# Performance work log

Measured on AMD Instinct MI355X. Metric: run time of the kernel, lower is better.

Reference implementation:

```python
import jax, jax.numpy as jnp
import numpy as np

B, L, S, T_IP = 2, 4096, 77, 16
C, C_CROSS, H = 1280, 768, 20
DH = C // H
REGION_WEIGHT = 0.3  # scalar inside weight_func: bias = region_state * sigma * REGION_WEIGHT
IP_SCALE = 1.0


def setup_inputs() -> dict:
    key = jax.random.key(0)
    ks = jax.random.split(key, 11)
    def w(k, shape, s=0.02):
        return jax.random.normal(k, shape, dtype=jnp.float32) * s
    return {
        "hidden_states": jax.random.normal(ks[0], (B, L, C), dtype=jnp.float32),
        "encoder_hidden_states": jax.random.normal(ks[1], (B, S, C_CROSS), dtype=jnp.float32),
        "ip_hidden_states": jax.random.normal(ks[2], (B, T_IP, C_CROSS), dtype=jnp.float32),
        "region_state": jax.random.uniform(ks[3], (B, L, S), dtype=jnp.float32),
        "sigma": jnp.full((1,), 14.6, dtype=jnp.float32),
        "Wq": w(ks[4], (C, C)),
        "Wk": w(ks[5], (C_CROSS, C)),
        "Wv": w(ks[6], (C_CROSS, C)),
        "Wk_ip": w(ks[7], (C_CROSS, C)),
        "Wv_ip": w(ks[8], (C_CROSS, C)),
        "Wout": w(ks[9], (C, C)),
        "b_out": jnp.zeros((C,), dtype=jnp.float32),
    }


def _split_heads(x):
    # [B, T, C] -> [B, H, T, DH]
    b, t, _ = x.shape
    return x.reshape(b, t, H, DH).transpose(0, 2, 1, 3)


def reference(hidden_states, encoder_hidden_states, ip_hidden_states, region_state,
              sigma, Wq, Wk, Wv, Wk_ip, Wv_ip, Wout, b_out):
    residual = hidden_states
    scale = 1.0 / np.sqrt(DH).astype(np.float32)

    q = _split_heads(hidden_states @ Wq)            # [B,H,L,DH]
    k = _split_heads(encoder_hidden_states @ Wk)    # [B,H,S,DH]
    v = _split_heads(encoder_hidden_states @ Wv)    # [B,H,S,DH]

    # region-state-biased cross attention (manual softmax path)
    scores = jnp.einsum('bhld,bhsd->bhls', q, k) * scale  # [B,H,L,S]
    # weight_func(region_state, sigma, attn_weight) -> region_state * sigma * REGION_WEIGHT,
    # broadcast over heads (repeat_interleave B -> B*H in the original).
    bias = (region_state * sigma[0] * REGION_WEIGHT)[:, None, :, :]  # [B,1,L,S]
    attn = jax.nn.softmax(scores + bias, axis=-1)
    out = jnp.einsum('bhls,bhsd->bhld', attn, v)
    out = out.transpose(0, 2, 1, 3).reshape(B, L, C)

    # IP-adapter stream: standard SDPA against image-prompt tokens
    k_ip = _split_heads(ip_hidden_states @ Wk_ip)   # [B,H,T,DH]
    v_ip = _split_heads(ip_hidden_states @ Wv_ip)
    s_ip = jax.nn.softmax(jnp.einsum('bhld,bhtd->bhlt', q, k_ip) * scale, axis=-1)
    out_ip = jnp.einsum('bhlt,bhtd->bhld', s_ip, v_ip).transpose(0, 2, 1, 3).reshape(B, L, C)

    out = out + IP_SCALE * out_ip
    out = out @ Wout + b_out     # attn.to_out[0]; to_out[1] is dropout (identity at p=0)
    return out + residual
```

## Files before the change

kernel.cpp:

```cpp
#include <hip/hip_runtime.h>
#include <cstdint>
#include <cstddef>

#define B_   2
#define L_   4096
#define S_   77
#define TIP_ 16
#define C_   1280
#define CC_  768
#define H_   20

typedef unsigned short u16;
typedef unsigned int   u32;
typedef __attribute__((ext_vector_type(8))) short bf16x8;
typedef __attribute__((ext_vector_type(8))) unsigned short u16x8;
typedef __attribute__((ext_vector_type(4))) float f32x4;

__device__ __forceinline__ u16 f2bf(float x) {
  u32 u = __float_as_uint(x);
  u32 r = (u + 0x7fffu + ((u >> 16) & 1u)) >> 16;
  return (u16)r;
}

__device__ __forceinline__ void gload16(const u16* g, const u16* l) {
  __builtin_amdgcn_global_load_lds(
      (const __attribute__((address_space(1))) u32*)g,
      (__attribute__((address_space(3))) u32*)(uintptr_t)l, 16, 0, 0);
}

__device__ __forceinline__ void wg_barrier() {
  asm volatile("s_barrier" ::: "memory");
}
template<int N>
__device__ __forceinline__ void vm_wait() {
  asm volatile("s_waitcnt vmcnt(%0)" :: "i"(N) : "memory");
}

__global__ __launch_bounds__(256) void prep_cast(
    const float* __restrict__ X, const float* __restrict__ enc, const float* __restrict__ ip,
    u16* __restrict__ Xbf, u16* __restrict__ encbf, u16* __restrict__ ipbf) {
  const int nX = B_*L_*C_;
  const int nE = B_*S_*CC_;
  const int nI = B_*TIP_*CC_;
  const int total4 = (nX + nE + nI) >> 2;
  for (int i = blockIdx.x*256 + threadIdx.x; i < total4; i += gridDim.x*256) {
    int idx = i << 2;
    const float* src; u16* dst; int off;
    if (idx < nX)            { src = X;   dst = Xbf;   off = idx; }
    else if (idx < nX + nE)  { src = enc; dst = encbf; off = idx - nX; }
    else                     { src = ip;  dst = ipbf;  off = idx - nX - nE; }
    float4 v = *(const float4*)(src + off);
    ushort4 o;
    o.x = f2bf(v.x); o.y = f2bf(v.y); o.z = f2bf(v.z); o.w = f2bf(v.w);
    *(ushort4*)(dst + off) = o;
  }
}

__global__ __launch_bounds__(256) void transpose_cast(
    const float* __restrict__ Wq,  const float* __restrict__ Wk,   const float* __restrict__ Wv,
    const float* __restrict__ Wkip,const float* __restrict__ Wvip, const float* __restrict__ Wout,
    u16* __restrict__ WqT, u16* __restrict__ WkT, u16* __restrict__ WvT,
    u16* __restrict__ WkipT, u16* __restrict__ WvipT, u16* __restrict__ WoutT) {
  const int m = blockIdx.y;
  const float* src; u16* dst; int K;
  switch (m) {
    case 0: src = Wq;   dst = WqT;   K = C_;  break;
    case 1: src = Wk;   dst = WkT;   K = CC_; break;
    case 2: src = Wv;   dst = WvT;   K = CC_; break;
    case 3: src = Wkip; dst = WkipT; K = CC_; break;
    case 4: src = Wvip; dst = WvipT; K = CC_; break;
    default:src = Wout; dst = WoutT; K = C_;  break;
  }
  const int tileK = blockIdx.x / 40;
  const int tileN = blockIdx.x % 40;
  if (tileK >= (K >> 5)) return;
  __shared__ float tile[32][33];
  const int tx = threadIdx.x & 31, ty = threadIdx.x >> 5;
  const int k0 = tileK*32, n0 = tileN*32;
  #pragma unroll
  for (int r = 0; r < 32; r += 8)
    tile[ty + r][tx] = src[(size_t)(k0 + ty + r)*C_ + n0 + tx];
  __syncthreads();
  #pragma unroll
  for (int r = 0; r < 32; r += 8) {
    const int n = n0 + ty + r, k = k0 + tx;
    dst[(size_t)n*K + k] = f2bf(tile[tx][ty + r]);
  }
}

template<int BN, int MODE, typename OutT>
__device__ __forceinline__ void gemm_core(
    const u16* __restrict__ A, int lda, int M,
    const u16* __restrict__ BT, int K,
    OutT* __restrict__ Cm,
    const float* __restrict__ bias, const float* __restrict__ resid,
    int mt, int nt) {
  constexpr int NF  = BN / 32;
  constexpr int BCH = BN / 32;
  constexpr int LP  = 4 + BCH;
  __shared__ u16 As0[128*64];
  __shared__ u16 Bs0[BN*64];
  __shared__ u16 As1[128*64];
  __shared__ u16 Bs1[BN*64];
  const int tid  = threadIdx.x;
  const int lane = tid & 63, wave = tid >> 6;
  const int wm = wave >> 1, wn = wave & 1;
  const int lhi = lane >> 4, llo = lane & 15;
  const int lsw = llo & 7;

  f32x4 acc[4][NF] = {};

  auto stage = [&](int kt, u16* As, u16* Bs) {
    #pragma unroll
    for (int it = 0; it < 4; ++it) {
      const int chunk = it*256 + wave*64 + lane;
      const int r  = chunk >> 3;
      const int c8 = chunk & 7;
      const int g8 = c8 ^ (r & 7);
      int row_g = mt*128 + r; row_g = (row_g < M) ? row_g : (M - 1);
      gload16(A + (size_t)row_g*lda + kt*64 + g8*8,
              As + (size_t)(it*256 + wave*64)*8);
    }
    #pragma unroll
    for (int it = 0; it < BCH; ++it) {
      const int chunk = it*256 + wave*64 + lane;
      const int r  = chunk >> 3;
      const int c8 = chunk & 7;
      const int g8 = c8 ^ (r & 7);
      const int nrow = nt*BN + r;
      gload16(BT + (size_t)nrow*K + kt*64 + g8*8,
              Bs + (size_t)(it*256 + wave*64)*8);
    }
  };

  auto compute = [&](const u16* As, const u16* Bs) {
    #pragma unroll
    for (int ks = 0; ks < 2; ++ks) {
      bf16x8 av[4], bv[NF];
      #pragma unroll
      for (int mm = 0; mm < 4; ++mm) {
        const int row = wm*64 + mm*16 + llo;
        av[mm] = *(const bf16x8*)(As + row*64 + (((ks*4 + lhi) ^ lsw) << 3));
      }
      #pragma unroll
      for (int nn = 0; nn < NF; ++nn) {
        const int row = wn*(BN/2) + nn*16 + llo;
        bv[nn] = *(const bf16x8*)(Bs + row*64 + (((ks*4 + lhi) ^ lsw) << 3));
      }
      #pragma unroll
      for (int mm = 0; mm < 4; ++mm)
        #pragma unroll
        for (int nn = 0; nn < NF; ++nn)
          acc[mm][nn] = __builtin_amdgcn_mfma_f32_16x16x32_bf16(av[mm], bv[nn], acc[mm][nn], 0, 0, 0);
    }
  };

  const int nkt = K >> 6;
  stage(0, As0, Bs0);
  stage(1, As1, Bs1);
  vm_wait<LP>();
  wg_barrier();
  __builtin_amdgcn_sched_barrier(0);

  for (int kt = 0; kt < nkt; ++kt) {
    u16* As = (kt & 1) ? As1 : As0;
    u16* Bs = (kt & 1) ? Bs1 : Bs0;
    compute(As, Bs);
    if (kt + 2 < nkt) {
      wg_barrier();
      stage(kt + 2, As, Bs);
      vm_wait<LP>();
      wg_barrier();
      __builtin_amdgcn_sched_barrier(0);
    } else if (kt + 1 < nkt) {
      vm_wait<0>();
      wg_barrier();
      __builtin_amdgcn_sched_barrier(0);
    }
  }

  #pragma unroll
  for (int mm = 0; mm < 4; ++mm) {
    #pragma unroll
    for (int nn = 0; nn < NF; ++nn) {
      const int row0 = mt*128 + wm*64 + mm*16 + lhi*4;
      const int col  = nt*BN + wn*(BN/2) + nn*16 + llo;
      #pragma unroll
      for (int r = 0; r < 4; ++r) {
        const int row = row0 + r;
        if (row < M) {
          float v = acc[mm][nn][r];
          if constexpr (MODE == 1) {
            v += bias[col] + resid[(size_t)row*C_ + col];
            Cm[(size_t)row*C_ + col] = v;
          } else {
            Cm[(size_t)row*C_ + col] = f2bf(v);
          }
        }
      }
    }
  }
}

template<int MODE, typename OutT>
__global__ __launch_bounds__(256, 2) void gemm_bf16(
    const u16* __restrict__ A, int lda, int M, const u16* __restrict__ BT, int K,
    OutT* __restrict__ Cm, const float* __restrict__ bias, const float* __restrict__ resid) {
  const int nwg = gridDim.x;
  const int bid = blockIdx.x;
  const int swz = (nwg & 7) ? bid : ((bid & 7) * (nwg >> 3) + (bid >> 3));
  gemm_core<160, MODE, OutT>(A, lda, M, BT, K, Cm, bias, resid, swz >> 3, swz & 7);
}

__global__ __launch_bounds__(256, 2) void gemm_small(
    const u16* __restrict__ encbf, const u16* __restrict__ ipbf,
    const u16* __restrict__ WkT, const u16* __restrict__ WvT,
    const u16* __restrict__ WkipT, const u16* __restrict__ WvipT,
    u16* __restrict__ Kbf, u16* __restrict__ Vbf,
    u16* __restrict__ Kipbf, u16* __restrict__ Vipbf) {
  const int z = blockIdx.y;
  const u16* A; const u16* BT; u16* Cm; int M;
  if      (z == 0) { A = encbf; BT = WkT;   Cm = Kbf;   M = B_*S_; }
  else if (z == 1) { A = encbf; BT = WvT;   Cm = Vbf;   M = B_*S_; }
  else if (z == 2) { A = ipbf;  BT = WkipT; Cm = Kipbf; M = B_*TIP_; }
  else             { A = ipbf;  BT = WvipT; Cm = Vipbf; M = B_*TIP_; }
  gemm_core<128, 2, u16>(A, CC_, M, BT, CC_, Cm, nullptr, nullptr, blockIdx.x / 10, blockIdx.x % 10);
}

#define KSP   96
#define KLD   72
#define PLD   104
__global__ __launch_bounds__(256) void attn_mfma(
    const u16* __restrict__ Qbf,
    const u16* __restrict__ Kbf,  const u16* __restrict__ Vbf,
    const u16* __restrict__ Kipbf, const u16* __restrict__ Vipbf,
    const float* __restrict__ region, const float* __restrict__ sigma,
    u16* __restrict__ attnbf) {
  __shared__ u16 Kl[KSP*KLD];
  __shared__ u16 Vt[64*PLD];
  __shared__ u16 Pl[4*32*PLD];
  const int b = blockIdx.z, h = blockIdx.y;
  const int tid = threadIdx.x, lane = tid & 63, wave = tid >> 6;
  const int llo = lane & 15, lhi = lane >> 4;

  for (int i = tid; i < KSP*8; i += 256) {
    const int r = i >> 3, c8 = i & 7;
    u16x8 val = {0,0,0,0,0,0,0,0};
    if (r < S_)
      val = *(const u16x8*)(Kbf + ((size_t)(b*S_ + r))*C_ + h*64 + c8*8);
    else if (r >= 80)
      val = *(const u16x8*)(Kipbf + ((size_t)(b*TIP_ + r - 80))*C_ + h*64 + c8*8);
    *(u16x8*)(Kl + r*KLD + c8*8) = val;
  }
  for (int i = tid; i < KSP*64; i += 256) {
    const int s = i >> 6, d = i & 63;
    u16 val = 0;
    if (s < S_)       val = Vbf[((size_t)(b*S_ + s))*C_ + h*64 + d];
    else if (s >= 80) val = Vipbf[((size_t)(b*TIP_ + s - 80))*C_ + h*64 + d];
    Vt[d*PLD + s] = val;
  }
  __syncthreads();

  const int row0 = blockIdx.x*128 + wave*32;

  bf16x8 av[2][2];
  #pragma unroll
  for (int mm = 0; mm < 2; ++mm)
    #pragma unroll
    for (int ks = 0; ks < 2; ++ks)
      av[mm][ks] = *(const bf16x8*)(Qbf + ((size_t)(b*L_ + row0 + mm*16 + llo))*C_ + h*64 + ks*32 + lhi*8);

  f32x4 acc[2][6] = {};
  #pragma unroll
  for (int ks = 0; ks < 2; ++ks) {
    bf16x8 bv[6];
    #pragma unroll
    for (int nn = 0; nn < 6; ++nn)
      bv[nn] = *(const bf16x8*)(Kl + (nn*16 + llo)*KLD + ks*32 + lhi*8);
    #pragma unroll
    for (int mm = 0; mm < 2; ++mm)
      #pragma unroll
      for (int nn = 0; nn < 6; ++nn)
        acc[mm][nn] = __builtin_amdgcn_mfma_f32_16x16x32_bf16(av[mm][ks], bv[nn], acc[mm][nn], 0, 0, 0);
  }

  const float sigscale = sigma[0] * 0.3f;
  const float scale = 0.125f;
  u16* Pw = Pl + wave*32*PLD;

  #pragma unroll
  for (int mm = 0; mm < 2; ++mm) {
    const int rowbase = b*L_ + row0 + mm*16 + lhi*4;
    float sc[5][4];
    float mx[4] = {-1e30f, -1e30f, -1e30f, -1e30f};
    #pragma unroll
    for (int nn = 0; nn < 5; ++nn) {
      const int col = nn*16 + llo;
      #pragma unroll
      for (int r = 0; r < 4; ++r) {
        float v = -1e30f;
        if (col < S_) {
          const float bias = region[((size_t)(rowbase + r))*S_ + col] * sigscale;
          v = fmaf(acc[mm][nn][r], scale, bias);
        }
        sc[nn][r] = v;
        mx[r] = fmaxf(mx[r], v);
      }
    }
    #pragma unroll
    for (int st = 1; st < 16; st <<= 1)
      #pragma unroll
      for (int r = 0; r < 4; ++r)
        mx[r] = fmaxf(mx[r], __shfl_xor(mx[r], st));
    float sum[4] = {0.f, 0.f, 0.f, 0.f};
    #pragma unroll
    for (int nn = 0; nn < 5; ++nn)
      #pragma unroll
      for (int r = 0; r < 4; ++r) {
        const float e = __expf(sc[nn][r] - mx[r]);
        sc[nn][r] = e; sum[r] += e;
      }
    #pragma unroll
    for (int st = 1; st < 16; st <<= 1)
      #pragma unroll
      for (int r = 0; r < 4; ++r)
        sum[r] += __shfl_xor(sum[r], st);
    float inv[4];
    #pragma unroll
    for (int r = 0; r < 4; ++r) inv[r] = 1.f / sum[r];

    float ipe[4], mi[4], sumi[4];
    #pragma unroll
    for (int r = 0; r < 4; ++r) { ipe[r] = acc[mm][5][r] * scale; mi[r] = ipe[r]; }
    #pragma unroll
    for (int st = 1; st < 16; st <<= 1)
      #pragma unroll
      for (int r = 0; r < 4; ++r)
        mi[r] = fmaxf(mi[r], __shfl_xor(mi[r], st));
    #pragma unroll
    for (int r = 0; r < 4; ++r) { ipe[r] = __expf(ipe[r] - mi[r]); sumi[r] = ipe[r]; }
    #pragma unroll
    for (int st = 1; st < 16; st <<= 1)
      #pragma unroll
      for (int r = 0; r < 4; ++r)
        sumi[r] += __shfl_xor(sumi[r], st);

    #pragma unroll
    for (int nn = 0; nn < 5; ++nn)
      #pragma unroll
      for (int r = 0; r < 4; ++r)
        Pw[(mm*16 + lhi*4 + r)*PLD + nn*16 + llo] = f2bf(sc[nn][r] * inv[r]);
    #pragma unroll
    for (int r = 0; r < 4; ++r)
      Pw[(mm*16 + lhi*4 + r)*PLD + 80 + llo] = f2bf(ipe[r] / sumi[r]);
  }

  f32x4 oacc[2][4] = {};
  #pragma unroll
  for (int ks = 0; ks < 3; ++ks) {
    bf16x8 pa[2], vv[4];
    #pragma unroll
    for (int mm = 0; mm < 2; ++mm)
      pa[mm] = *(const bf16x8*)(Pw + (mm*16 + llo)*PLD + ks*32 + lhi*8);
    #pragma unroll
    for (int nn = 0; nn < 4; ++nn)
      vv[nn] = *(const bf16x8*)(Vt + (nn*16 + llo)*PLD + ks*32 + lhi*8);
    #pragma unroll
    for (int mm = 0; mm < 2; ++mm)
      #pragma unroll
      for (int nn = 0; nn < 4; ++nn)
        oacc[mm][nn] = __builtin_amdgcn_mfma_f32_16x16x32_bf16(pa[mm], vv[nn], oacc[mm][nn], 0, 0, 0);
  }

  #pragma unroll
  for (int mm = 0; mm < 2; ++mm)
    #pragma unroll
    for (int nn = 0; nn < 4; ++nn)
      #pragma unroll
      for (int r = 0; r < 4; ++r) {
        const int grow = row0 + mm*16 + lhi*4 + r;
        attnbf[((size_t)(b*L_ + grow))*C_ + h*64 + nn*16 + llo] = f2bf(oacc[mm][nn][r]);
      }
}

extern "C" void kernel_launch(void* const* d_in, const int* in_sizes, int n_in,
                              void* d_out, int out_size, void* d_ws, size_t ws_size,
                              hipStream_t stream) {
  const float* hidden = (const float*)d_in[0];
  const float* enc    = (const float*)d_in[1];
  const float* ip     = (const float*)d_in[2];
  const float* region = (const float*)d_in[3];
  const float* sigma  = (const float*)d_in[4];
  const float* Wq     = (const float*)d_in[5];
  const float* Wk     = (const float*)d_in[6];
  const float* Wv     = (const float*)d_in[7];
  const float* Wkip   = (const float*)d_in[8];
  const float* Wvip   = (const float*)d_in[9];
  const float* Wout   = (const float*)d_in[10];
  const float* bout   = (const float*)d_in[11];

  char* base = (char*)d_ws;
  size_t off = 0;
  auto carve = [&](size_t bytes) -> void* {
    void* r = base + off;
    off += (bytes + 255) & ~(size_t)255;
    return r;
  };
  u16* Xbf    = (u16*)carve((size_t)B_*L_*C_*2);
  u16* encbf  = (u16*)carve((size_t)B_*S_*CC_*2);
  u16* ipbf   = (u16*)carve((size_t)B_*TIP_*CC_*2);
  u16* WqT    = (u16*)carve((size_t)C_*C_*2);
  u16* WkT    = (u16*)carve((size_t)C_*CC_*2);
  u16* WvT    = (u16*)carve((size_t)C_*CC_*2);
  u16* WkipT  = (u16*)carve((size_t)C_*CC_*2);
  u16* WvipT  = (u16*)carve((size_t)C_*CC_*2);
  u16* WoutT  = (u16*)carve((size_t)C_*C_*2);
  u16* Qbf    = (u16*)carve((size_t)B_*L_*C_*2);
  u16* Kbf    = (u16*)carve((size_t)B_*S_*C_*2);
  u16* Vbf    = (u16*)carve((size_t)B_*S_*C_*2);
  u16* Kipbf  = (u16*)carve((size_t)B_*TIP_*C_*2);
  u16* Vipbf  = (u16*)carve((size_t)B_*TIP_*C_*2);
  u16* attnbf = (u16*)carve((size_t)B_*L_*C_*2);
  (void)ws_size; (void)in_sizes; (void)n_in; (void)out_size;

  prep_cast<<<2048, 256, 0, stream>>>(hidden, enc, ip, Xbf, encbf, ipbf);
  transpose_cast<<<dim3(1600, 6), 256, 0, stream>>>(Wq, Wk, Wv, Wkip, Wvip, Wout,
                                                    WqT, WkT, WvT, WkipT, WvipT, WoutT);
  gemm_bf16<2, u16><<<dim3(512), 256, 0, stream>>>(Xbf, C_, B_*L_, WqT, C_, Qbf, nullptr, nullptr);
  gemm_small<<<dim3(2*10, 4), 256, 0, stream>>>(encbf, ipbf, WkT, WvT, WkipT, WvipT,
                                                Kbf, Vbf, Kipbf, Vipbf);
  attn_mfma<<<dim3(L_/128, H_, B_), 256, 0, stream>>>(Qbf, Kbf, Vbf, Kipbf, Vipbf,
                                                      region, sigma, attnbf);
  gemm_bf16<1, float><<<dim3(512), 256, 0, stream>>>(attnbf, C_, B_*L_, WoutT, C_,
                                                     (float*)d_out, bout, hidden);
}
```

Before: 150.8 us.

## Use 4-stage BK=32 GEMM pipeline, merge prep kernels, retile small GEMM

The GEMM core changes from a double-buffered K=64 tile to a four-buffer ring of K=32 tiles with three loads in flight. This drops one barrier per iteration and uses a new XOR swizzle. The two preprocessing kernels (activation cast and weight transpose-cast) become one launch with a flat block index, which also removes the early-exit blocks of the old 2D grid. The small K/V projection GEMM now uses the fixed 160-wide tile over 48 blocks. Together these aim to hide memory latency better and cut launch overhead, at the cost of more barrier-bound K-steps and a single buffer-reuse barrier.

```diff
diff --git a/kernel.cpp b/kernel.cpp
--- a/kernel.cpp
+++ b/kernel.cpp
@@ -36,45 +36,42 @@
   asm volatile("s_waitcnt vmcnt(%0)" :: "i"(N) : "memory");
 }
 
-__global__ __launch_bounds__(256) void prep_cast(
+__global__ __launch_bounds__(256) void prep_all(
     const float* __restrict__ X, const float* __restrict__ enc, const float* __restrict__ ip,
-    u16* __restrict__ Xbf, u16* __restrict__ encbf, u16* __restrict__ ipbf) {
-  const int nX = B_*L_*C_;
-  const int nE = B_*S_*CC_;
-  const int nI = B_*TIP_*CC_;
-  const int total4 = (nX + nE + nI) >> 2;
-  for (int i = blockIdx.x*256 + threadIdx.x; i < total4; i += gridDim.x*256) {
-    int idx = i << 2;
-    const float* src; u16* dst; int off;
-    if (idx < nX)            { src = X;   dst = Xbf;   off = idx; }
-    else if (idx < nX + nE)  { src = enc; dst = encbf; off = idx - nX; }
-    else                     { src = ip;  dst = ipbf;  off = idx - nX - nE; }
-    float4 v = *(const float4*)(src + off);
-    ushort4 o;
-    o.x = f2bf(v.x); o.y = f2bf(v.y); o.z = f2bf(v.z); o.w = f2bf(v.w);
-    *(ushort4*)(dst + off) = o;
-  }
-}
-
-__global__ __launch_bounds__(256) void transpose_cast(
+    u16* __restrict__ Xbf, u16* __restrict__ encbf, u16* __restrict__ ipbf,
     const float* __restrict__ Wq,  const float* __restrict__ Wk,   const float* __restrict__ Wv,
     const float* __restrict__ Wkip,const float* __restrict__ Wvip, const float* __restrict__ Wout,
     u16* __restrict__ WqT, u16* __restrict__ WkT, u16* __restrict__ WvT,
     u16* __restrict__ WkipT, u16* __restrict__ WvipT, u16* __restrict__ WoutT) {
-  const int m = blockIdx.y;
+  __shared__ float tile[32][33];
+  const int bid = blockIdx.x;
+  if (bid < 2048) {
+    const int nX = B_*L_*C_;
+    const int nE = B_*S_*CC_;
+    const int nI = B_*TIP_*CC_;
+    const int total4 = (nX + nE + nI) >> 2;
+    for (int i = bid*256 + threadIdx.x; i < total4; i += 2048*256) {
+      int idx = i << 2;
+      const float* src; u16* dst; int off;
+      if (idx < nX)            { src = X;   dst = Xbf;   off = idx; }
+      else if (idx < nX + nE)  { src = enc; dst = encbf; off = idx - nX; }
+      else                     { src = ip;  dst = ipbf;  off = idx - nX - nE; }
+      float4 v = *(const float4*)(src + off);
+      ushort4 o;
+      o.x = f2bf(v.x); o.y = f2bf(v.y); o.z = f2bf(v.z); o.w = f2bf(v.w);
+      *(ushort4*)(dst + off) = o;
+    }
+    return;
+  }
+  int t = bid - 2048;
   const float* src; u16* dst; int K;
-  switch (m) {
-    case 0: src = Wq;   dst = WqT;   K = C_;  break;
-    case 1: src = Wk;   dst = WkT;   K = CC_; break;
-    case 2: src = Wv;   dst = WvT;   K = CC_; break;
-    case 3: src = Wkip; dst = WkipT; K = CC_; break;
-    case 4: src = Wvip; dst = WvipT; K = CC_; break;
-    default:src = Wout; dst = WoutT; K = C_;  break;
-  }
-  const int tileK = blockIdx.x / 40;
-  const int tileN = blockIdx.x % 40;
-  if (tileK >= (K >> 5)) return;
-  __shared__ float tile[32][33];
+  if      (t < 1600) { src = Wq;   dst = WqT;   K = C_;  }
+  else if (t < 2560) { src = Wk;   dst = WkT;   K = CC_; t -= 1600; }
+  else if (t < 3520) { src = Wv;   dst = WvT;   K = CC_; t -= 2560; }
+  else if (t < 4480) { src = Wkip; dst = WkipT; K = CC_; t -= 3520; }
+  else if (t < 5440) { src = Wvip; dst = WvipT; K = CC_; t -= 4480; }
+  else               { src = Wout; dst = WoutT; K = C_;  t -= 5440; }
+  const int tileK = t / 40, tileN = t % 40;
   const int tx = threadIdx.x & 31, ty = threadIdx.x >> 5;
   const int k0 = tileK*32, n0 = tileN*32;
   #pragma unroll
@@ -88,103 +85,97 @@
   }
 }
 
-template<int BN, int MODE, typename OutT>
+template<int MODE, typename OutT>
 __device__ __forceinline__ void gemm_core(
     const u16* __restrict__ A, int lda, int M,
     const u16* __restrict__ BT, int K,
     OutT* __restrict__ Cm,
     const float* __restrict__ bias, const float* __restrict__ resid,
     int mt, int nt) {
-  constexpr int NF  = BN / 32;
-  constexpr int BCH = BN / 32;
-  constexpr int LP  = 4 + BCH;
-  __shared__ u16 As0[128*64];
-  __shared__ u16 Bs0[BN*64];
-  __shared__ u16 As1[128*64];
-  __shared__ u16 Bs1[BN*64];
+  __shared__ u16 As[4][128*32];
+  __shared__ u16 Bs[4][160*32];
   const int tid  = threadIdx.x;
   const int lane = tid & 63, wave = tid >> 6;
   const int wm = wave >> 1, wn = wave & 1;
   const int lhi = lane >> 4, llo = lane & 15;
-  const int lsw = llo & 7;
-
-  f32x4 acc[4][NF] = {};
-
-  auto stage = [&](int kt, u16* As, u16* Bs) {
-    #pragma unroll
-    for (int it = 0; it < 4; ++it) {
+
+  f32x4 acc[4][5] = {};
+
+  auto stage = [&](int kt) {
+    u16* Asb = As[kt & 3];
+    u16* Bsb = Bs[kt & 3];
+    #pragma unroll
+    for (int it = 0; it < 2; ++it) {
       const int chunk = it*256 + wave*64 + lane;
-      const int r  = chunk >> 3;
-      const int c8 = chunk & 7;
-      const int g8 = c8 ^ (r & 7);
+      const int r = chunk >> 2, c = chunk & 3;
+      const int g = c ^ ((r >> 1) & 3);
       int row_g = mt*128 + r; row_g = (row_g < M) ? row_g : (M - 1);
-      gload16(A + (size_t)row_g*lda + kt*64 + g8*8,
-              As + (size_t)(it*256 + wave*64)*8);
-    }
-    #pragma unroll
-    for (int it = 0; it < BCH; ++it) {
+      gload16(A + (size_t)row_g*lda + kt*32 + g*8,
+              Asb + (size_t)(it*256 + wave*64)*8);
+    }
+    #pragma unroll
+    for (int it = 0; it < 2; ++it) {
       const int chunk = it*256 + wave*64 + lane;
-      const int r  = chunk >> 3;
-      const int c8 = chunk & 7;
-      const int g8 = c8 ^ (r & 7);
-      const int nrow = nt*BN + r;
-      gload16(BT + (size_t)nrow*K + kt*64 + g8*8,
-              Bs + (size_t)(it*256 + wave*64)*8);
+      const int r = chunk >> 2, c = chunk & 3;
+      const int g = c ^ ((r >> 1) & 3);
+      const int nrow = nt*160 + r;
+      gload16(BT + (size_t)nrow*K + kt*32 + g*8,
+              Bsb + (size_t)(it*256 + wave*64)*8);
+    }
+    { const int chunk = 512 + (wave & 1)*64 + lane;
+      const int r = chunk >> 2, c = chunk & 3;
+      const int g = c ^ ((r >> 1) & 3);
+      const int nrow = nt*160 + r;
+      gload16(BT + (size_t)nrow*K + kt*32 + g*8,
+              Bsb + (size_t)(512 + (wave & 1)*64)*8);
     }
   };
 
-  auto compute = [&](const u16* As, const u16* Bs) {
-    #pragma unroll
-    for (int ks = 0; ks < 2; ++ks) {
-      bf16x8 av[4], bv[NF];
-      #pragma unroll
-      for (int mm = 0; mm < 4; ++mm) {
-        const int row = wm*64 + mm*16 + llo;
-        av[mm] = *(const bf16x8*)(As + row*64 + (((ks*4 + lhi) ^ lsw) << 3));
-      }
-      #pragma unroll
-      for (int nn = 0; nn < NF; ++nn) {
-        const int row = wn*(BN/2) + nn*16 + llo;
-        bv[nn] = *(const bf16x8*)(Bs + row*64 + (((ks*4 + lhi) ^ lsw) << 3));
-      }
-      #pragma unroll
-      for (int mm = 0; mm < 4; ++mm)
-        #pragma unroll
-        for (int nn = 0; nn < NF; ++nn)
-          acc[mm][nn] = __builtin_amdgcn_mfma_f32_16x16x32_bf16(av[mm], bv[nn], acc[mm][nn], 0, 0, 0);
-    }
+  auto compute = [&](int kt) {
+    const u16* Asb = As[kt & 3];
+    const u16* Bsb = Bs[kt & 3];
+    bf16x8 av[4], bv[5];
+    #pragma unroll
+    for (int mm = 0; mm < 4; ++mm) {
+      const int row = wm*64 + mm*16 + llo;
+      av[mm] = *(const bf16x8*)(Asb + row*32 + ((lhi ^ ((row >> 1) & 3)) << 3));
+    }
+    #pragma unroll
+    for (int nn = 0; nn < 5; ++nn) {
+      const int row = wn*80 + nn*16 + llo;
+      bv[nn] = *(const bf16x8*)(Bsb + row*32 + ((lhi ^ ((row >> 1) & 3)) << 3));
+    }
+    #pragma unroll
+    for (int mm = 0; mm < 4; ++mm)
+      #pragma unroll
+      for (int nn = 0; nn < 5; ++nn)
+        acc[mm][nn] = __builtin_amdgcn_mfma_f32_16x16x32_bf16(av[mm], bv[nn], acc[mm][nn], 0, 0, 0);
   };
 
-  const int nkt = K >> 6;
-  stage(0, As0, Bs0);
-  stage(1, As1, Bs1);
-  vm_wait<LP>();
+  const int nkt = K >> 5;
+  stage(0); stage(1); stage(2);
+  vm_wait<10>();
   wg_barrier();
-  __builtin_amdgcn_sched_barrier(0);
 
   for (int kt = 0; kt < nkt; ++kt) {
-    u16* As = (kt & 1) ? As1 : As0;
-    u16* Bs = (kt & 1) ? Bs1 : Bs0;
-    compute(As, Bs);
-    if (kt + 2 < nkt) {
-      wg_barrier();
-      stage(kt + 2, As, Bs);
-      vm_wait<LP>();
-      wg_barrier();
-      __builtin_amdgcn_sched_barrier(0);
-    } else if (kt + 1 < nkt) {
+    compute(kt);
+    if (kt + 3 < nkt) {
+      stage(kt + 3);
+      vm_wait<10>();
+    } else if (kt + 2 < nkt) {
+      vm_wait<5>();
+    } else {
       vm_wait<0>();
-      wg_barrier();
-      __builtin_amdgcn_sched_barrier(0);
-    }
+    }
+    wg_barrier();
   }
 
   #pragma unroll
   for (int mm = 0; mm < 4; ++mm) {
     #pragma unroll
-    for (int nn = 0; nn < NF; ++nn) {
+    for (int nn = 0; nn < 5; ++nn) {
       const int row0 = mt*128 + wm*64 + mm*16 + lhi*4;
-      const int col  = nt*BN + wn*(BN/2) + nn*16 + llo;
+      const int col  = nt*160 + wn*80 + nn*16 + llo;
       #pragma unroll
       for (int r = 0; r < 4; ++r) {
         const int row = row0 + r;
@@ -209,7 +200,7 @@
   const int nwg = gridDim.x;
   const int bid = blockIdx.x;
   const int swz = (nwg & 7) ? bid : ((bid & 7) * (nwg >> 3) + (bid >> 3));
-  gemm_core<160, MODE, OutT>(A, lda, M, BT, K, Cm, bias, resid, swz >> 3, swz & 7);
+  gemm_core<MODE, OutT>(A, lda, M, BT, K, Cm, bias, resid, swz >> 3, swz & 7);
 }
 
 __global__ __launch_bounds__(256, 2) void gemm_small(
@@ -218,13 +209,17 @@
     const u16* __restrict__ WkipT, const u16* __restrict__ WvipT,
     u16* __restrict__ Kbf, u16* __restrict__ Vbf,
     u16* __restrict__ Kipbf, u16* __restrict__ Vipbf) {
-  const int z = blockIdx.y;
-  const u16* A; const u16* BT; u16* Cm; int M;
-  if      (z == 0) { A = encbf; BT = WkT;   Cm = Kbf;   M = B_*S_; }
-  else if (z == 1) { A = encbf; BT = WvT;   Cm = Vbf;   M = B_*S_; }
-  else if (z == 2) { A = ipbf;  BT = WkipT; Cm = Kipbf; M = B_*TIP_; }
-  else             { A = ipbf;  BT = WvipT; Cm = Vipbf; M = B_*TIP_; }
-  gemm_core<128, 2, u16>(A, CC_, M, BT, CC_, Cm, nullptr, nullptr, blockIdx.x / 10, blockIdx.x % 10);
+  const int zr = blockIdx.x >> 3, nt = blockIdx.x & 7;
+  const u16* A; const u16* BT; u16* Cm; int M, mt;
+  switch (zr) {
+    case 0: A = encbf; BT = WkT;   Cm = Kbf;   M = B_*S_;   mt = 0; break;
+    case 1: A = encbf; BT = WkT;   Cm = Kbf;   M = B_*S_;   mt = 1; break;
+    case 2: A = encbf; BT = WvT;   Cm = Vbf;   M = B_*S_;   mt = 0; break;
+    case 3: A = encbf; BT = WvT;   Cm = Vbf;   M = B_*S_;   mt = 1; break;
+    case 4: A = ipbf;  BT = WkipT; Cm = Kipbf; M = B_*TIP_; mt = 0; break;
+    default:A = ipbf;  BT = WvipT; Cm = Vipbf; M = B_*TIP_; mt = 0; break;
+  }
+  gemm_core<2, u16>(A, CC_, M, BT, CC_, Cm, nullptr, nullptr, mt, nt);
 }
 
 #define KSP   96
@@ -423,12 +418,13 @@
   u16* attnbf = (u16*)carve((size_t)B_*L_*C_*2);
   (void)ws_size; (void)in_sizes; (void)n_in; (void)out_size;
 
-  prep_cast<<<2048, 256, 0, stream>>>(hidden, enc, ip, Xbf, encbf, ipbf);
-  transpose_cast<<<dim3(1600, 6), 256, 0, stream>>>(Wq, Wk, Wv, Wkip, Wvip, Wout,
-                                                    WqT, WkT, WvT, WkipT, WvipT, WoutT);
+  prep_all<<<dim3(2048 + 7040), 256, 0, stream>>>(
+      hidden, enc, ip, Xbf, encbf, ipbf,
+      Wq, Wk, Wv, Wkip, Wvip, Wout,
+      WqT, WkT, WvT, WkipT, WvipT, WoutT);
   gemm_bf16<2, u16><<<dim3(512), 256, 0, stream>>>(Xbf, C_, B_*L_, WqT, C_, Qbf, nullptr, nullptr);
-  gemm_small<<<dim3(2*10, 4), 256, 0, stream>>>(encbf, ipbf, WkT, WvT, WkipT, WvipT,
-                                                Kbf, Vbf, Kipbf, Vipbf);
+  gemm_small<<<dim3(48), 256, 0, stream>>>(encbf, ipbf, WkT, WvT, WkipT, WvipT,
+                                           Kbf, Vbf, Kipbf, Vipbf);
   attn_mfma<<<dim3(L_/128, H_, B_), 256, 0, stream>>>(Qbf, Kbf, Vbf, Kipbf, Vipbf,
                                                       region, sigma, attnbf);
   gemm_bf16<1, float><<<dim3(512), 256, 0, stream>>>(attnbf, C_, B_*L_, WoutT, C_,
```

Result: slower. 162.7 us (+7.9%).
